# Optimization experiments

Hardware: AMD Instinct MI355X
Metric: run time of the kernel (lower is better)

The kernel has to match this reference:

```python
import jax, jax.numpy as jnp
import numpy as np

N_NODES = 50000
N_EDGES = 1600000
D_FEAT = 64
N_SCALARS = 4
N_GRAPHS = 64
HIDDEN = 128
OUT = 128


def setup_inputs() -> dict:
    key = jax.random.key(0)
    ks = jax.random.split(key, 8)
    x = jax.random.normal(ks[0], (N_NODES, D_FEAT), dtype=jnp.float32)
    scalars = jax.random.normal(ks[1], (N_GRAPHS, N_SCALARS), dtype=jnp.float32)
    batch = jnp.sort(jax.random.randint(ks[2], (N_NODES,), 0, N_GRAPHS))
    edge_index = jax.random.randint(ks[3], (2, N_EDGES), 0, N_NODES)
    d_in = 2 * (D_FEAT + N_SCALARS)  # 136: EdgeConv-style cat([x_i, x_j - x_i])
    W1 = jax.random.normal(ks[4], (d_in, HIDDEN), dtype=jnp.float32) * (1.0 / np.sqrt(d_in))
    b1 = jnp.zeros((HIDDEN,), dtype=jnp.float32)
    W2 = jax.random.normal(ks[5], (HIDDEN, OUT), dtype=jnp.float32) * (1.0 / np.sqrt(HIDDEN))
    b2 = jnp.zeros((OUT,), dtype=jnp.float32)
    return {"x": x, "scalars": scalars, "batch": batch, "edge_index": edge_index,
            "W1": W1, "b1": b1, "W2": W2, "b2": b2}


def reference(x, scalars, batch, edge_index, W1, b1, W2, b2):
    # _reshape_scalars: gather per-graph scalars to nodes via batch index
    s = scalars[batch]                       # [N, n_scalars]
    h = jnp.concatenate([x, s], axis=-1)     # [N, d_feat + n_scalars]
    src, dst = edge_index[0], edge_index[1]  # edge j -> i (PyG convention)
    h_i = h[dst]                             # target node features [E, F]
    h_j = h[src]                             # source node features [E, F]
    m_in = jnp.concatenate([h_i, h_j - h_i], axis=-1)  # [E, 2F]
    m = jax.nn.relu(m_in @ W1 + b1) @ W2 + b2          # edge MLP [E, OUT]
    out = jax.ops.segment_sum(m, dst, num_segments=x.shape[0])  # add-aggregation
    return out
```

## Files before the change

kernel.cpp:

```cpp
#include <hip/hip_runtime.h>

#define N_NODES   50000
#define N_EDGES   1600000
#define D_FEAT    64
#define N_SCALARS 4
#define HIDDEN    128
#define OUT_DIM   128
#define UV_DIM    256

#define SLICE_SH  6
#define SLICE_N   (1 << SLICE_SH)
#define NSLICE    ((N_NODES + SLICE_N - 1) >> SLICE_SH)
#define CAP       2560
#define CAPN      80
#define CAPN_DW   (CAPN / 2)
#define CHUNK     4096
#define SENTINEL  50000
#define SRC_HALF  25000

#define N_WAVES   (N_NODES / 16)
#define G1_BLOCKS ((N_WAVES + 3) / 4)
#define BIN_BLOCKS ((N_EDGES + CHUNK - 1) / CHUNK)
#define AGG_BLOCKS (N_NODES / 16)

typedef __attribute__((ext_vector_type(8))) _Float16 half8;
typedef __attribute__((ext_vector_type(2))) _Float16 half2v;
typedef __attribute__((ext_vector_type(4))) float    f32x4;

__device__ __forceinline__ float wf_elem(const float* W1, int k, int j) {
    float wb = W1[(k + 68) * HIDDEN + (j & 127)];
    return (j < HIDDEN) ? (W1[k * HIDDEN + j] - wb) : wb;
}

__device__ __forceinline__ unsigned char f2bf8(float f) {
    unsigned short h = __builtin_bit_cast(unsigned short, (_Float16)f);
    unsigned r = ((unsigned)h + 0x7Fu + ((h >> 8) & 1u)) >> 8;
    return (unsigned char)r;
}

__device__ __forceinline__ half2v bf8lo(unsigned v) {
    return __builtin_bit_cast(half2v, __builtin_amdgcn_perm(0u, v, 0x010C000Cu));
}
__device__ __forceinline__ half2v bf8hi(unsigned v) {
    return __builtin_bit_cast(half2v, __builtin_amdgcn_perm(0u, v, 0x030C020Cu));
}
__device__ __forceinline__ half2v h2bc(unsigned v) {
    return __builtin_bit_cast(half2v, v);
}
__device__ __forceinline__ unsigned h2u(half2v v) {
    return __builtin_bit_cast(unsigned, v);
}

__global__ __launch_bounds__(256) void prep_kernel(
    const float* __restrict__ W1, const float* __restrict__ b1,
    const float* __restrict__ W2, const float* __restrict__ scalars,
    _Float16* __restrict__ WfT, _Float16* __restrict__ W2T,
    float* __restrict__ SG, int* __restrict__ tails,
    unsigned char* __restrict__ Vb8)
{
    const int idx = blockIdx.x * 256 + threadIdx.x;
    {   int j = idx >> 6, k = idx & 63;
        WfT[idx] = (_Float16)wf_elem(W1, k, j); }
    {   int j = idx >> 7, k = idx & 127;
        W2T[idx] = (_Float16)W2[k * OUT_DIM + j]; }
    {   int g = idx >> 8, j = idx & 255;
        float s = (j < HIDDEN) ? b1[j] : 0.f;
        #pragma unroll
        for (int t = 0; t < N_SCALARS; ++t)
            s = fmaf(scalars[g * N_SCALARS + t], wf_elem(W1, D_FEAT + t, j), s);
        SG[idx] = s; }
    if (idx < NSLICE) tails[idx] = 0;
    if (idx < 32)
        ((unsigned*)(Vb8 + (size_t)SENTINEL * HIDDEN))[idx] = 0xFCFCFCFCu;
}

__global__ __launch_bounds__(256) void gemm1_bin(
    const float* __restrict__ x, const int* __restrict__ batch,
    const _Float16* __restrict__ WfT, const float* __restrict__ SG,
    _Float16* __restrict__ Uh, unsigned char* __restrict__ Vb8,
    const int* __restrict__ ei, int* __restrict__ tails,
    unsigned* __restrict__ glist)
{
    __shared__ unsigned buf[CHUNK];
    __shared__ int hist[NSLICE];
    __shared__ int binStart[NSLICE];
    __shared__ int cursor[NSLICE];
    __shared__ int gbase[NSLICE];
    __shared__ int scanTmp[256];

    const int tid = threadIdx.x;

    if (blockIdx.x < G1_BLOCKS) {
        const int wid = (blockIdx.x * 256 + tid) >> 6;
        if (wid >= N_WAVES) return;
        const int lane = tid & 63;
        const int quad = lane >> 4;
        const int l15  = lane & 15;
        const int row0 = wid * 16;

        f32x4 acc[16];
        #pragma unroll
        for (int c = 0; c < 16; ++c) { f32x4 z = {0.f,0.f,0.f,0.f}; acc[c] = z; }

        const float* xrow = x + (row0 + l15) * D_FEAT;
        #pragma unroll
        for (int t = 0; t < 2; ++t) {
            const int k0 = 32 * t + quad * 8;
            float4 a0 = *(const float4*)(xrow + k0);
            float4 a1 = *(const float4*)(xrow + k0 + 4);
            half8 af;
            af[0] = (_Float16)a0.x; af[1] = (_Float16)a0.y;
            af[2] = (_Float16)a0.z; af[3] = (_Float16)a0.w;
            af[4] = (_Float16)a1.x; af[5] = (_Float16)a1.y;
            af[6] = (_Float16)a1.z; af[7] = (_Float16)a1.w;
            #pragma unroll
            for (int c = 0; c < 16; ++c) {
                half8 bf = *(const half8*)(WfT + (c * 16 + l15) * 64 + k0);
                acc[c] = __builtin_amdgcn_mfma_f32_16x16x32_f16(af, bf, acc[c], 0, 0, 0);
            }
        }

        const int gA = batch[row0];
        const int gB = batch[row0 + 15];

        if (gA == gB) {
            const float* SGr = SG + gA * UV_DIM;
            #pragma unroll
            for (int c = 0; c < 16; ++c) {
                const int col = c * 16 + l15;
                const float sg = SGr[col];
                #pragma unroll
                for (int j = 0; j < 4; ++j) {
                    const int n = row0 + quad * 4 + j;
                    float v = acc[c][j] + sg;
                    if (col < HIDDEN) Uh[(n << 7) + col] = (_Float16)v;
                    else              Vb8[(n << 7) + col - HIDDEN] = f2bf8(v);
                }
            }
        } else {
            int bg[4];
            #pragma unroll
            for (int j = 0; j < 4; ++j) bg[j] = batch[row0 + quad * 4 + j];
            #pragma unroll
            for (int c = 0; c < 16; ++c) {
                const int col = c * 16 + l15;
                #pragma unroll
                for (int j = 0; j < 4; ++j) {
                    const int n = row0 + quad * 4 + j;
                    float v = acc[c][j] + SG[bg[j] * UV_DIM + col];
                    if (col < HIDDEN) Uh[(n << 7) + col] = (_Float16)v;
                    else              Vb8[(n << 7) + col - HIDDEN] = f2bf8(v);
                }
            }
        }
        return;
    }

    const int e0  = (blockIdx.x - G1_BLOCKS) * CHUNK;
    const int nE  = min(CHUNK, N_EDGES - e0);

    for (int i = tid; i < NSLICE; i += 256) hist[i] = 0;
    __syncthreads();

    unsigned ent[CHUNK / 256];
    #pragma unroll
    for (int j = 0; j < CHUNK / 256; ++j) {
        int e = e0 + tid + j * 256;
        if (e < N_EDGES) {
            unsigned s = (unsigned)ei[e];
            unsigned d = (unsigned)ei[N_EDGES + e];
            ent[j] = (d << 16) | s;
            atomicAdd(&hist[d >> SLICE_SH], 1);
        } else {
            ent[j] = 0xFFFFFFFFu;
        }
    }
    __syncthreads();

    const int base4 = tid * 4;
    int loc[4];
    int sum = 0;
    #pragma unroll
    for (int k = 0; k < 4; ++k) {
        int b = base4 + k;
        loc[k] = (b < NSLICE) ? hist[b] : 0;
        sum += loc[k];
    }
    scanTmp[tid] = sum;
    __syncthreads();
    for (int d = 1; d < 256; d <<= 1) {
        int v = (tid >= d) ? scanTmp[tid - d] : 0;
        __syncthreads();
        scanTmp[tid] += v;
        __syncthreads();
    }
    int run = (tid == 0) ? 0 : scanTmp[tid - 1];
    #pragma unroll
    for (int k = 0; k < 4; ++k) {
        int b = base4 + k;
        if (b < NSLICE) { binStart[b] = run; cursor[b] = run; run += loc[k]; }
    }
    __syncthreads();

    #pragma unroll
    for (int j = 0; j < CHUNK / 256; ++j) {
        if (ent[j] != 0xFFFFFFFFu) {
            int sl = (int)(ent[j] >> (16 + SLICE_SH));
            int pos = atomicAdd(&cursor[sl], 1);
            buf[pos] = ent[j];
        }
    }
    __syncthreads();

    for (int s = tid; s < NSLICE; s += 256) {
        int c = hist[s];
        if (c > 0) gbase[s] = atomicAdd(&tails[s], c);
    }
    __syncthreads();

    for (int i = tid; i < nE; i += 256) {
        unsigned e = buf[i];
        int sl = (int)(e >> (16 + SLICE_SH));
        int di = gbase[sl] + (i - binStart[sl]);
        if (di < CAP) glist[(size_t)sl * CAP + di] = e;
    }
}

__global__ __launch_bounds__(256) void rebin_kernel(
    const unsigned* glist, const int* __restrict__ tails,
    unsigned short* nlist, int* __restrict__ degN)
{
    __shared__ unsigned short lists[64 * CAPN];
    __shared__ int cur[64];

    const int sl  = blockIdx.x;
    const int tid = threadIdx.x;
    const unsigned* lst = glist + (size_t)sl * CAP;
    const int cnt = min(tails[sl], CAP);

    unsigned* L32 = (unsigned*)lists;
    #pragma unroll
    for (int k = 0; k < (64 * CAPN_DW) / 256; ++k)
        L32[tid + k * 256] = (SENTINEL << 16) | SENTINEL;
    if (tid < 64) cur[tid] = 0;
    __syncthreads();

    for (int i = tid; i < cnt; i += 256) {
        unsigned e = lst[i];
        if ((e & 0xFFFFu) < SRC_HALF) {
            int b = (e >> 16) & 63;
            int pos = atomicAdd(&cur[b], 1);
            if (pos < CAPN) lists[b * CAPN + pos] = (unsigned short)e;
        }
    }
    __syncthreads();
    for (int i = tid; i < cnt; i += 256) {
        unsigned e = lst[i];
        if ((e & 0xFFFFu) >= SRC_HALF) {
            int b = (e >> 16) & 63;
            int pos = atomicAdd(&cur[b], 1);
            if (pos < CAPN) lists[b * CAPN + pos] = (unsigned short)e;
        }
    }
    __syncthreads();

    unsigned* N32 = (unsigned*)nlist + (size_t)sl * (64 * CAPN_DW);
    #pragma unroll
    for (int k = 0; k < (64 * CAPN_DW) / 256; ++k)
        N32[tid + k * 256] = L32[tid + k * 256];

    if (tid < 64) degN[sl * 64 + tid] = min(cur[tid], CAPN);
}

__global__ __launch_bounds__(256) void agg_gemm2(
    const unsigned short* __restrict__ nlist, const int* __restrict__ degN,
    const _Float16* __restrict__ Uh, const unsigned char* __restrict__ Vb8,
    const _Float16* __restrict__ W2T, const float* __restrict__ b2,
    float* __restrict__ out)
{
    __shared__ _Float16 aggA[16][136];
    __shared__ int deg16[16];

    const int node0 = blockIdx.x << 4;
    const int tid   = threadIdx.x;
    const int wave  = tid >> 6;
    const int lane  = tid & 63;
    const int g     = lane >> 3;
    const int co    = (lane & 7) * 16;
    const half2v zero = {(_Float16)0, (_Float16)0};

    if (tid < 16) deg16[tid] = min(degN[node0 + tid], CAPN);

    const int nbase = node0 + wave * 4;
    int dg[4];
    #pragma unroll
    for (int i = 0; i < 4; ++i) dg[i] = min(degN[nbase + i], CAPN);
    const int nch = (max(max(dg[0], dg[1]), max(dg[2], dg[3])) + 7) >> 3;

    const unsigned char* Vbc = Vb8 + co;
    const unsigned short* Lp[4];
    #pragma unroll
    for (int i = 0; i < 4; ++i)
        Lp[i] = nlist + (size_t)(nbase + i) * CAPN + g;

    half2v U[4][8], A[4][8];
    #pragma unroll
    for (int i = 0; i < 4; ++i) {
        const _Float16* up = Uh + (((size_t)(nbase + i)) << 7) + co;
        uint4 a = *(const uint4*)up;
        uint4 b = *(const uint4*)(up + 8);
        U[i][0] = h2bc(a.x); U[i][1] = h2bc(a.y);
        U[i][2] = h2bc(a.z); U[i][3] = h2bc(a.w);
        U[i][4] = h2bc(b.x); U[i][5] = h2bc(b.y);
        U[i][6] = h2bc(b.z); U[i][7] = h2bc(b.w);
        #pragma unroll
        for (int k = 0; k < 8; ++k) A[i][k] = zero;
    }

    unsigned sidc[4];
    #pragma unroll
    for (int i = 0; i < 4; ++i) sidc[i] = Lp[i][0];

    for (int ch = 0; ch < nch; ++ch) {
        uint4 v[4];
        #pragma unroll
        for (int i = 0; i < 4; ++i)
            v[i] = *(const uint4*)(Vbc + ((size_t)sidc[i] << 7));
        unsigned sidn[4];
        #pragma unroll
        for (int i = 0; i < 4; ++i) sidn[i] = Lp[i][(ch + 1) * 8];
        #pragma unroll
        for (int i = 0; i < 4; ++i) {
            A[i][0] += __builtin_elementwise_max(U[i][0] + bf8lo(v[i].x), zero);
            A[i][1] += __builtin_elementwise_max(U[i][1] + bf8hi(v[i].x), zero);
            A[i][2] += __builtin_elementwise_max(U[i][2] + bf8lo(v[i].y), zero);
            A[i][3] += __builtin_elementwise_max(U[i][3] + bf8hi(v[i].y), zero);
            A[i][4] += __builtin_elementwise_max(U[i][4] + bf8lo(v[i].z), zero);
            A[i][5] += __builtin_elementwise_max(U[i][5] + bf8hi(v[i].z), zero);
            A[i][6] += __builtin_elementwise_max(U[i][6] + bf8lo(v[i].w), zero);
            A[i][7] += __builtin_elementwise_max(U[i][7] + bf8hi(v[i].w), zero);
            sidc[i] = sidn[i];
        }
    }

    #pragma unroll
    for (int i = 0; i < 4; ++i) {
        #pragma unroll
        for (int k = 0; k < 8; ++k) {
            half2v t = A[i][k];
            t += h2bc((unsigned)__shfl_xor((int)h2u(t), 8));
            t += h2bc((unsigned)__shfl_xor((int)h2u(t), 16));
            t += h2bc((unsigned)__shfl_xor((int)h2u(t), 32));
            A[i][k] = t;
        }
    }

    if (lane < 8) {
        #pragma unroll
        for (int i = 0; i < 4; ++i) {
            _Float16* dst = &aggA[wave * 4 + i][co];
            uint4 w0 = { h2u(A[i][0]), h2u(A[i][1]), h2u(A[i][2]), h2u(A[i][3]) };
            uint4 w1 = { h2u(A[i][4]), h2u(A[i][5]), h2u(A[i][6]), h2u(A[i][7]) };
            *(uint4*)dst = w0;
            *(uint4*)(dst + 8) = w1;
        }
    }
    __syncthreads();

    const int quad = lane >> 4;
    const int l15  = lane & 15;
    f32x4 accm[2];
    {   f32x4 z = {0.f,0.f,0.f,0.f}; accm[0] = z; accm[1] = z; }
    #pragma unroll
    for (int t = 0; t < 4; ++t) {
        const int k0 = 32 * t + quad * 8;
        half8 af = *(const half8*)&aggA[l15][k0];
        #pragma unroll
        for (int c = 0; c < 2; ++c) {
            const int ct = wave * 2 + c;
            half8 bf = *(const half8*)(W2T + ((ct * 16 + l15) << 7) + k0);
            accm[c] = __builtin_amdgcn_mfma_f32_16x16x32_f16(af, bf, accm[c], 0, 0, 0);
        }
    }
    int dgj[4];
    #pragma unroll
    for (int j = 0; j < 4; ++j) dgj[j] = deg16[quad * 4 + j];

    #pragma unroll
    for (int c = 0; c < 2; ++c) {
        const int col = (wave * 2 + c) * 16 + l15;
        const float bb = b2[col];
        #pragma unroll
        for (int j = 0; j < 4; ++j) {
            const int n = node0 + quad * 4 + j;
            out[(size_t)n * OUT_DIM + col] = accm[c][j] + bb * (float)dgj[j];
        }
    }
}

extern "C" void kernel_launch(void* const* d_in, const int* in_sizes, int n_in,
                              void* d_out, int out_size, void* d_ws, size_t ws_size,
                              hipStream_t stream)
{
    const float* x       = (const float*)d_in[0];
    const float* scalars = (const float*)d_in[1];
    const int*   batch   = (const int*)d_in[2];
    const int*   ei      = (const int*)d_in[3];
    const float* W1      = (const float*)d_in[4];
    const float* b1      = (const float*)d_in[5];
    const float* W2      = (const float*)d_in[6];
    const float* b2      = (const float*)d_in[7];
    float*       out     = (float*)d_out;

    _Float16*       Uh    = (_Float16*)d_ws;
    unsigned char*  Vb8   = (unsigned char*)(Uh + (size_t)N_NODES * HIDDEN);
    unsigned*       glist = (unsigned*)(Vb8 + (size_t)(N_NODES + 1) * HIDDEN);
    unsigned short* nlist = (unsigned short*)glist;
    int*            degN  = (int*)(glist + (size_t)NSLICE * CAP);
    _Float16*       WfT   = (_Float16*)(degN + NSLICE * SLICE_N);
    _Float16*       W2T   = WfT + 256 * 64;
    float*          SG    = (float*)(W2T + 128 * 128);
    int*            tails = (int*)(SG + 64 * UV_DIM);

    prep_kernel<<<64, 256, 0, stream>>>(W1, b1, W2, scalars, WfT, W2T, SG, tails, Vb8);

    gemm1_bin<<<G1_BLOCKS + BIN_BLOCKS, 256, 0, stream>>>(
        x, batch, WfT, SG, Uh, Vb8, ei, tails, glist);

    rebin_kernel<<<NSLICE, 256, 0, stream>>>(glist, tails, nlist, degN);

    agg_gemm2<<<AGG_BLOCKS, 256, 0, stream>>>(
        nlist, degN, Uh, Vb8, W2T, b2, out);
}
```

Measured before the change: 168.5 us.

## Use 8 waves per aggregation block with 2 nodes each; single-pass rebin

The aggregation+GEMM2 kernel now launches 512 threads (8 waves) per 16-node block. Each wave gathers for 2 nodes instead of 4 and computes one 16-column MFMA tile instead of two. This is meant to raise parallelism and occupancy and to cut per-wave register pressure for the latency-bound gather. Separately, the rebin kernel drops its two-pass split by source half and fills the lists in a single pass. That removes a barrier and a second read of the list, but it gives up the source-ordering that may have helped cache locality in the gather.

```diff
diff --git a/kernel.cpp b/kernel.cpp
--- a/kernel.cpp
+++ b/kernel.cpp
@@ -247,20 +247,9 @@
 
     for (int i = tid; i < cnt; i += 256) {
         unsigned e = lst[i];
-        if ((e & 0xFFFFu) < SRC_HALF) {
-            int b = (e >> 16) & 63;
-            int pos = atomicAdd(&cur[b], 1);
-            if (pos < CAPN) lists[b * CAPN + pos] = (unsigned short)e;
-        }
-    }
-    __syncthreads();
-    for (int i = tid; i < cnt; i += 256) {
-        unsigned e = lst[i];
-        if ((e & 0xFFFFu) >= SRC_HALF) {
-            int b = (e >> 16) & 63;
-            int pos = atomicAdd(&cur[b], 1);
-            if (pos < CAPN) lists[b * CAPN + pos] = (unsigned short)e;
-        }
+        int b = (e >> 16) & 63;
+        int pos = atomicAdd(&cur[b], 1);
+        if (pos < CAPN) lists[b * CAPN + pos] = (unsigned short)e;
     }
     __syncthreads();
 
@@ -272,7 +261,7 @@
     if (tid < 64) degN[sl * 64 + tid] = min(cur[tid], CAPN);
 }
 
-__global__ __launch_bounds__(256) void agg_gemm2(
+__global__ __launch_bounds__(512, 8) void agg_gemm2(
     const unsigned short* __restrict__ nlist, const int* __restrict__ degN,
     const _Float16* __restrict__ Uh, const unsigned char* __restrict__ Vb8,
     const _Float16* __restrict__ W2T, const float* __restrict__ b2,
@@ -291,110 +280,106 @@
 
     if (tid < 16) deg16[tid] = min(degN[node0 + tid], CAPN);
 
-    const int nbase = node0 + wave * 4;
-    int dg[4];
-    #pragma unroll
-    for (int i = 0; i < 4; ++i) dg[i] = min(degN[nbase + i], CAPN);
-    const int nch = (max(max(dg[0], dg[1]), max(dg[2], dg[3])) + 7) >> 3;
+    const int n0 = node0 + wave * 2;
+    const int d0 = min(degN[n0], CAPN);
+    const int d1 = min(degN[n0 + 1], CAPN);
+    const int nch = (max(d0, d1) + 7) >> 3;
 
     const unsigned char* Vbc = Vb8 + co;
-    const unsigned short* Lp[4];
-    #pragma unroll
-    for (int i = 0; i < 4; ++i)
-        Lp[i] = nlist + (size_t)(nbase + i) * CAPN + g;
-
-    half2v U[4][8], A[4][8];
-    #pragma unroll
-    for (int i = 0; i < 4; ++i) {
-        const _Float16* up = Uh + (((size_t)(nbase + i)) << 7) + co;
+    const unsigned short* L0 = nlist + (size_t)n0 * CAPN + g;
+    const unsigned short* L1 = L0 + CAPN;
+
+    half2v U0[8], U1[8], A0[8], A1[8];
+    {
+        const _Float16* up = Uh + (((size_t)n0) << 7) + co;
         uint4 a = *(const uint4*)up;
         uint4 b = *(const uint4*)(up + 8);
-        U[i][0] = h2bc(a.x); U[i][1] = h2bc(a.y);
-        U[i][2] = h2bc(a.z); U[i][3] = h2bc(a.w);
-        U[i][4] = h2bc(b.x); U[i][5] = h2bc(b.y);
-        U[i][6] = h2bc(b.z); U[i][7] = h2bc(b.w);
+        U0[0] = h2bc(a.x); U0[1] = h2bc(a.y);
+        U0[2] = h2bc(a.z); U0[3] = h2bc(a.w);
+        U0[4] = h2bc(b.x); U0[5] = h2bc(b.y);
+        U0[6] = h2bc(b.z); U0[7] = h2bc(b.w);
+        uint4 c = *(const uint4*)(up + 128);
+        uint4 d = *(const uint4*)(up + 136);
+        U1[0] = h2bc(c.x); U1[1] = h2bc(c.y);
+        U1[2] = h2bc(c.z); U1[3] = h2bc(c.w);
+        U1[4] = h2bc(d.x); U1[5] = h2bc(d.y);
+        U1[6] = h2bc(d.z); U1[7] = h2bc(d.w);
         #pragma unroll
-        for (int k = 0; k < 8; ++k) A[i][k] = zero;
-    }
-
-    unsigned sidc[4];
-    #pragma unroll
-    for (int i = 0; i < 4; ++i) sidc[i] = Lp[i][0];
-
+        for (int k = 0; k < 8; ++k) { A0[k] = zero; A1[k] = zero; }
+    }
+
+    unsigned s0 = L0[0], s1 = L1[0];
     for (int ch = 0; ch < nch; ++ch) {
-        uint4 v[4];
-        #pragma unroll
-        for (int i = 0; i < 4; ++i)
-            v[i] = *(const uint4*)(Vbc + ((size_t)sidc[i] << 7));
-        unsigned sidn[4];
-        #pragma unroll
-        for (int i = 0; i < 4; ++i) sidn[i] = Lp[i][(ch + 1) * 8];
-        #pragma unroll
-        for (int i = 0; i < 4; ++i) {
-            A[i][0] += __builtin_elementwise_max(U[i][0] + bf8lo(v[i].x), zero);
-            A[i][1] += __builtin_elementwise_max(U[i][1] + bf8hi(v[i].x), zero);
-            A[i][2] += __builtin_elementwise_max(U[i][2] + bf8lo(v[i].y), zero);
-            A[i][3] += __builtin_elementwise_max(U[i][3] + bf8hi(v[i].y), zero);
-            A[i][4] += __builtin_elementwise_max(U[i][4] + bf8lo(v[i].z), zero);
-            A[i][5] += __builtin_elementwise_max(U[i][5] + bf8hi(v[i].z), zero);
-            A[i][6] += __builtin_elementwise_max(U[i][6] + bf8lo(v[i].w), zero);
-            A[i][7] += __builtin_elementwise_max(U[i][7] + bf8hi(v[i].w), zero);
-            sidc[i] = sidn[i];
-        }
-    }
-
-    #pragma unroll
-    for (int i = 0; i < 4; ++i) {
-        #pragma unroll
-        for (int k = 0; k < 8; ++k) {
-            half2v t = A[i][k];
-            t += h2bc((unsigned)__shfl_xor((int)h2u(t), 8));
-            t += h2bc((unsigned)__shfl_xor((int)h2u(t), 16));
-            t += h2bc((unsigned)__shfl_xor((int)h2u(t), 32));
-            A[i][k] = t;
-        }
+        uint4 v0 = *(const uint4*)(Vbc + ((size_t)s0 << 7));
+        uint4 v1 = *(const uint4*)(Vbc + ((size_t)s1 << 7));
+        s0 = L0[(ch + 1) * 8];
+        s1 = L1[(ch + 1) * 8];
+        A0[0] += __builtin_elementwise_max(U0[0] + bf8lo(v0.x), zero);
+        A0[1] += __builtin_elementwise_max(U0[1] + bf8hi(v0.x), zero);
+        A0[2] += __builtin_elementwise_max(U0[2] + bf8lo(v0.y), zero);
+        A0[3] += __builtin_elementwise_max(U0[3] + bf8hi(v0.y), zero);
+        A0[4] += __builtin_elementwise_max(U0[4] + bf8lo(v0.z), zero);
+        A0[5] += __builtin_elementwise_max(U0[5] + bf8hi(v0.z), zero);
+        A0[6] += __builtin_elementwise_max(U0[6] + bf8lo(v0.w), zero);
+        A0[7] += __builtin_elementwise_max(U0[7] + bf8hi(v0.w), zero);
+        A1[0] += __builtin_elementwise_max(U1[0] + bf8lo(v1.x), zero);
+        A1[1] += __builtin_elementwise_max(U1[1] + bf8hi(v1.x), zero);
+        A1[2] += __builtin_elementwise_max(U1[2] + bf8lo(v1.y), zero);
+        A1[3] += __builtin_elementwise_max(U1[3] + bf8hi(v1.y), zero);
+        A1[4] += __builtin_elementwise_max(U1[4] + bf8lo(v1.z), zero);
+        A1[5] += __builtin_elementwise_max(U1[5] + bf8hi(v1.z), zero);
+        A1[6] += __builtin_elementwise_max(U1[6] + bf8lo(v1.w), zero);
+        A1[7] += __builtin_elementwise_max(U1[7] + bf8hi(v1.w), zero);
+    }
+
+    #pragma unroll
+    for (int k = 0; k < 8; ++k) {
+        half2v t0 = A0[k];
+        t0 += h2bc((unsigned)__shfl_xor((int)h2u(t0), 8));
+        t0 += h2bc((unsigned)__shfl_xor((int)h2u(t0), 16));
+        t0 += h2bc((unsigned)__shfl_xor((int)h2u(t0), 32));
+        A0[k] = t0;
+        half2v t1 = A1[k];
+        t1 += h2bc((unsigned)__shfl_xor((int)h2u(t1), 8));
+        t1 += h2bc((unsigned)__shfl_xor((int)h2u(t1), 16));
+        t1 += h2bc((unsigned)__shfl_xor((int)h2u(t1), 32));
+        A1[k] = t1;
     }
 
     if (lane < 8) {
-        #pragma unroll
-        for (int i = 0; i < 4; ++i) {
-            _Float16* dst = &aggA[wave * 4 + i][co];
-            uint4 w0 = { h2u(A[i][0]), h2u(A[i][1]), h2u(A[i][2]), h2u(A[i][3]) };
-            uint4 w1 = { h2u(A[i][4]), h2u(A[i][5]), h2u(A[i][6]), h2u(A[i][7]) };
-            *(uint4*)dst = w0;
-            *(uint4*)(dst + 8) = w1;
-        }
+        _Float16* dst0 = &aggA[wave * 2][co];
+        uint4 w0 = { h2u(A0[0]), h2u(A0[1]), h2u(A0[2]), h2u(A0[3]) };
+        uint4 w1 = { h2u(A0[4]), h2u(A0[5]), h2u(A0[6]), h2u(A0[7]) };
+        *(uint4*)dst0 = w0;
+        *(uint4*)(dst0 + 8) = w1;
+        _Float16* dst1 = &aggA[wave * 2 + 1][co];
+        uint4 w2 = { h2u(A1[0]), h2u(A1[1]), h2u(A1[2]), h2u(A1[3]) };
+        uint4 w3 = { h2u(A1[4]), h2u(A1[5]), h2u(A1[6]), h2u(A1[7]) };
+        *(uint4*)dst1 = w2;
+        *(uint4*)(dst1 + 8) = w3;
     }
     __syncthreads();
 
     const int quad = lane >> 4;
     const int l15  = lane & 15;
-    f32x4 accm[2];
-    {   f32x4 z = {0.f,0.f,0.f,0.f}; accm[0] = z; accm[1] = z; }
+    f32x4 accm = {0.f, 0.f, 0.f, 0.f};
     #pragma unroll
     for (int t = 0; t < 4; ++t) {
         const int k0 = 32 * t + quad * 8;
         half8 af = *(const half8*)&aggA[l15][k0];
-        #pragma unroll
-        for (int c = 0; c < 2; ++c) {
-            const int ct = wave * 2 + c;
-            half8 bf = *(const half8*)(W2T + ((ct * 16 + l15) << 7) + k0);
-            accm[c] = __builtin_amdgcn_mfma_f32_16x16x32_f16(af, bf, accm[c], 0, 0, 0);
-        }
+        half8 bf = *(const half8*)(W2T + ((wave * 16 + l15) << 7) + k0);
+        accm = __builtin_amdgcn_mfma_f32_16x16x32_f16(af, bf, accm, 0, 0, 0);
     }
     int dgj[4];
     #pragma unroll
     for (int j = 0; j < 4; ++j) dgj[j] = deg16[quad * 4 + j];
 
-    #pragma unroll
-    for (int c = 0; c < 2; ++c) {
-        const int col = (wave * 2 + c) * 16 + l15;
-        const float bb = b2[col];
-        #pragma unroll
-        for (int j = 0; j < 4; ++j) {
-            const int n = node0 + quad * 4 + j;
-            out[(size_t)n * OUT_DIM + col] = accm[c][j] + bb * (float)dgj[j];
-        }
+    const int col = wave * 16 + l15;
+    const float bb = b2[col];
+    #pragma unroll
+    for (int j = 0; j < 4; ++j) {
+        const int n = node0 + quad * 4 + j;
+        out[(size_t)n * OUT_DIM + col] = accm[j] + bb * (float)dgj[j];
     }
 }
 
@@ -429,6 +414,6 @@
 
     rebin_kernel<<<NSLICE, 256, 0, stream>>>(glist, tails, nlist, degN);
 
-    agg_gemm2<<<AGG_BLOCKS, 256, 0, stream>>>(
+    agg_gemm2<<<AGG_BLOCKS, 512, 0, stream>>>(
         nlist, degN, Uh, Vb8, W2T, b2, out);
 }
```

New measurement: 167.5 us. About the same (-0.6%).
